# Performance work log

Measured on AMD Instinct MI355X. Metric: run time of the kernel, lower is better.

The kernel has to match this reference:

```python
import jax, jax.numpy as jnp
import numpy as np

SPATIAL_SHAPES = ((64, 64), (32, 32), (16, 16), (8, 8))  # (H_l, W_l) per level
N_HEADS, N_LEVELS, N_POINTS = 8, 4, 4
EMBED, HEAD_DIM = 256, 32


def _bilinear_sample(v_lvl, loc, H, W):
    """grid_sample(mode=bilinear, padding=zeros, align_corners=False).

    v_lvl: (B, nH, H*W, d)   loc: (B, Nq, nH, P, 2) with (x, y) in [0, 1].
    Returns (B, nH, Nq, P, d).
    """
    B, nH, _, d = v_lvl.shape
    Nq, P = loc.shape[1], loc.shape[3]
    g = 2.0 * loc - 1.0                      # normalized [-1, 1]
    px = ((g[..., 0] + 1.0) * W - 1.0) * 0.5  # pixel coords, align_corners=False
    py = ((g[..., 1] + 1.0) * H - 1.0) * 0.5
    x0 = jnp.floor(px); y0 = jnp.floor(py)
    wx = px - x0; wy = py - y0
    x0i = x0.astype(jnp.int32); y0i = y0.astype(jnp.int32)
    acc = jnp.zeros((B, nH, Nq * P, d), v_lvl.dtype)
    corners = ((0, 0, (1 - wx) * (1 - wy)), (1, 0, wx * (1 - wy)),
               (0, 1, (1 - wx) * wy), (1, 1, wx * wy))
    for dx, dy, w in corners:
        xi = x0i + dx; yi = y0i + dy
        valid = (xi >= 0) & (xi < W) & (yi >= 0) & (yi < H)
        idx = jnp.clip(yi, 0, H - 1) * W + jnp.clip(xi, 0, W - 1)  # (B,Nq,nH,P)
        idx_t = idx.transpose(0, 2, 1, 3).reshape(B, nH, Nq * P)
        wm = jnp.where(valid, w, 0.0).astype(v_lvl.dtype)
        wm = wm.transpose(0, 2, 1, 3).reshape(B, nH, Nq * P, 1)
        gathered = jnp.take_along_axis(v_lvl, idx_t[..., None], axis=2)
        acc = acc + wm * gathered
    return acc.reshape(B, nH, Nq, P, d)


def setup_inputs() -> dict:
    key = jax.random.key(0)
    ks = jax.random.split(key, 12)
    B, Nq = 4, sum(H * W for H, W in SPATIAL_SHAPES)
    Nv = Nq
    s = 1.0 / np.sqrt(EMBED)
    return {
        "query": jax.random.normal(ks[0], (B, Nq, EMBED), jnp.float32),
        "value": jax.random.normal(ks[1], (B, Nv, EMBED), jnp.float32),
        "reference_points": jax.random.uniform(ks[2], (B, Nq, N_LEVELS, 2), jnp.float32),
        "value_proj_w": jax.random.normal(ks[3], (EMBED, EMBED), jnp.float32) * s,
        "value_proj_b": jnp.zeros((EMBED,), jnp.float32),
        "offsets_w": jax.random.normal(ks[4], (EMBED, N_HEADS * N_LEVELS * N_POINTS * 2), jnp.float32) * (0.05 * s),
        "offsets_b": jax.random.normal(ks[5], (N_HEADS * N_LEVELS * N_POINTS * 2,), jnp.float32) * 2.0,
        "attn_w_w": jax.random.normal(ks[6], (EMBED, N_HEADS * N_LEVELS * N_POINTS), jnp.float32) * s,
        "attn_w_b": jnp.zeros((N_HEADS * N_LEVELS * N_POINTS,), jnp.float32),
        "out_w": jax.random.normal(ks[7], (EMBED, EMBED), jnp.float32) * s,
        "out_b": jnp.zeros((EMBED,), jnp.float32),
    }


def reference(query, value, reference_points, value_proj_w, value_proj_b,
              offsets_w, offsets_b, attn_w_w, attn_w_b, out_w, out_b):
    B, Nq, C = query.shape
    Nv = value.shape[1]
    v = (value @ value_proj_w + value_proj_b).reshape(B, Nv, N_HEADS, HEAD_DIM)
    off = (query @ offsets_w + offsets_b).reshape(B, Nq, N_HEADS, N_LEVELS, N_POINTS, 2)
    aw = (query @ attn_w_w + attn_w_b).reshape(B, Nq, N_HEADS, N_LEVELS * N_POINTS)
    aw = jax.nn.softmax(aw, axis=-1).reshape(B, Nq, N_HEADS, N_LEVELS, N_POINTS)
    norm = jnp.array([[W, H] for H, W in SPATIAL_SHAPES], dtype=query.dtype)  # (L,2) as (W,H)
    loc = reference_points[:, :, None, :, None, :] + off / norm[None, None, None, :, None, :]
    out = jnp.zeros((B, Nq, N_HEADS, HEAD_DIM), query.dtype)
    cursor = 0
    for l, (H, W) in enumerate(SPATIAL_SHAPES):
        v_lvl = v[:, cursor:cursor + H * W].transpose(0, 2, 1, 3)  # (B,nH,HW,d)
        cursor += H * W
        sampled = _bilinear_sample(v_lvl, loc[:, :, :, l], H, W)   # (B,nH,Nq,P,d)
        out = out + jnp.einsum('bnhp,bhnpd->bnhd', aw[:, :, :, l], sampled)
    return out.reshape(B, Nq, C) @ out_w + out_b
```

## Files before the change

kernel.cpp:

```cpp
#include <hip/hip_runtime.h>
#include <hip/hip_bf16.h>
#include <math.h>

#define B_ 4
#define NQ 5440
#define M_ROWS (B_ * NQ)
#define NH 8
#define NL 4
#define NP 4
#define HD 32

typedef __attribute__((ext_vector_type(8))) short bf16x8;
typedef __attribute__((ext_vector_type(4))) short bf16x4;
typedef __attribute__((ext_vector_type(4))) float f32x4;
typedef _Float16 f16;

static __device__ __forceinline__ unsigned short f2bf(float f) {
  union { float f; unsigned u; } v; v.f = f;
  unsigned r = (v.u + 0x7fffu + ((v.u >> 16) & 1u)) >> 16;
  return (unsigned short)r;
}
static __device__ __forceinline__ float bits2f(unsigned u) {
  union { unsigned u; float f; } v; v.u = u; return v.f;
}

__global__ __launch_bounds__(256) void prep_all(
    const float* __restrict__ value, const float* __restrict__ query,
    unsigned short* __restrict__ value_bf, unsigned short* __restrict__ query_bf,
    const float* __restrict__ vpw, const float* __restrict__ offw,
    const float* __restrict__ attnw, const float* __restrict__ outw,
    const float* __restrict__ offb, const float* __restrict__ attnb,
    unsigned short* __restrict__ vp_t, unsigned short* __restrict__ q_t,
    unsigned short* __restrict__ out_t, float* __restrict__ biasq, int n4) {
  int id = blockIdx.x * 256 + threadIdx.x;
  if (id < 2 * n4) {
    const float* src; unsigned short* dst; int j;
    if (id < n4) { src = value; dst = value_bf; j = id; }
    else { src = query; dst = query_bf; j = id - n4; }
    float4 f = ((const float4*)src)[j];
    bf16x4 o;
    o[0] = (short)f2bf(f.x); o[1] = (short)f2bf(f.y);
    o[2] = (short)f2bf(f.z); o[3] = (short)f2bf(f.w);
    ((bf16x4*)dst)[j] = o;
    return;
  }
  int w = id - 2 * n4;
  if (w < 65536) {
    int n = w >> 8, k = w & 255;
    vp_t[w] = f2bf(vpw[k * 256 + n]);
  } else if (w < 163840) {
    int q = w - 65536; int n = q >> 8, k = q & 255;
    q_t[q] = f2bf(n < 256 ? offw[k * 256 + n] : attnw[k * 128 + (n - 256)]);
  } else if (w < 229376) {
    int o = w - 163840; int n = o >> 8, k = o & 255;
    out_t[o] = f2bf(outw[k * 256 + n]);
  } else if (w < 229760) {
    int j = w - 229376;
    biasq[j] = j < 256 ? offb[j] : attnb[j - 256];
  }
}

__global__ __launch_bounds__(256) void gemm12_kernel(
    const unsigned short* __restrict__ valbf, const unsigned short* __restrict__ qrybf,
    const unsigned short* __restrict__ wt_vp, const unsigned short* __restrict__ wt_q,
    const float* __restrict__ vp_b, const float* __restrict__ biasq,
    unsigned short* __restrict__ v_bf, f16* __restrict__ offaw_h) {
  __shared__ unsigned short Bs[8 * 64 * 32];
  const int t = threadIdx.x;
  const int lane = t & 63, wid = t >> 6;
  const int qd = lane >> 4, l16 = lane & 15;
  const int g = blockIdx.x;
  const int grp = g / 80, r = g % 80;
  int by, bx;
  if (grp < 21) { by = grp * 8 + (r & 7); bx = r >> 3; }
  else          { by = 168 + (r & 1);     bx = r >> 1; }
  const int bm = by * 128;
  const bool isv = bx < 4;
  const int bn = isv ? bx * 64 : (bx - 4) * 64;
  const unsigned short* A  = isv ? valbf : qrybf;
  const unsigned short* Wt = isv ? wt_vp : wt_q;

  const unsigned short* bg = Wt + (size_t)(bn + (t >> 2)) * 256 + (t & 3) * 8;
  unsigned short* bs_b = Bs + (t & 192) * 8;
#pragma unroll
  for (int j = 0; j < 8; ++j)
    __builtin_amdgcn_global_load_lds(
        (const __attribute__((address_space(1))) void*)(bg + j * 32),
        (__attribute__((address_space(3))) void*)(bs_b + j * 2048), 16, 0, 0);

  const unsigned short* ar0 = A + (size_t)(bm + wid * 32 + l16) * 256 + qd * 8;
  const unsigned short* ar1 = ar0 + 16 * 256;
  bf16x8 a0[8], a1[8];
#pragma unroll
  for (int j = 0; j < 8; ++j) {
    a0[j] = *(const bf16x8*)(ar0 + j * 32);
    a1[j] = *(const bf16x8*)(ar1 + j * 32);
  }
  __syncthreads();

  f32x4 acc[2][4] = {};
#pragma unroll
  for (int j = 0; j < 8; ++j) {
    const unsigned short* bt = Bs + j * 2048 + l16 * 32 + qd * 8;
#pragma unroll
    for (int ni = 0; ni < 4; ++ni) {
      const bf16x8 bf = *(const bf16x8*)(bt + ni * 512);
      acc[0][ni] = __builtin_amdgcn_mfma_f32_16x16x32_bf16(a0[j], bf, acc[0][ni], 0, 0, 0);
      acc[1][ni] = __builtin_amdgcn_mfma_f32_16x16x32_bf16(a1[j], bf, acc[1][ni], 0, 0, 0);
    }
  }
  if (isv) {
#pragma unroll
    for (int ni = 0; ni < 4; ++ni) {
      const int c = bn + ni * 16 + l16;
      const float bb = vp_b[c];
      const int h = c >> 5, d = c & 31;
#pragma unroll
      for (int mi = 0; mi < 2; ++mi)
#pragma unroll
        for (int rr = 0; rr < 4; ++rr) {
          const int gm = bm + wid * 32 + mi * 16 + qd * 4 + rr;
          const int b = gm / NQ, pix = gm - b * NQ;
          v_bf[((size_t)(b * NH + h) * NQ + pix) * HD + d] = f2bf(acc[mi][ni][rr] + bb);
        }
    }
  } else {
#pragma unroll
    for (int ni = 0; ni < 4; ++ni) {
      const int c = bn + ni * 16 + l16;
      const float bb = biasq[c];
#pragma unroll
      for (int mi = 0; mi < 2; ++mi)
#pragma unroll
        for (int rr = 0; rr < 4; ++rr) {
          const int gm = bm + wid * 32 + mi * 16 + qd * 4 + rr;
          offaw_h[(size_t)gm * 384 + c] = (f16)(acc[mi][ni][rr] + bb);
        }
    }
  }
}

__global__ __launch_bounds__(256) void gemm_out_kernel(
    const unsigned short* __restrict__ attn_bf, const unsigned short* __restrict__ wt_out,
    const float* __restrict__ out_b, float* __restrict__ out) {
  __shared__ unsigned short Bs[8 * 64 * 32];
  const int t = threadIdx.x;
  const int lane = t & 63, wid = t >> 6;
  const int qd = lane >> 4, l16 = lane & 15;
  const int g = blockIdx.x;
  const int grp = g / 32, r = g % 32;
  int by, bx;
  if (grp < 21) { by = grp * 8 + (r & 7); bx = r >> 3; }
  else          { by = 168 + (r & 1);     bx = r >> 1; }
  const int bm = by * 128, bn = bx * 64;

  const unsigned short* bg = wt_out + (size_t)(bn + (t >> 2)) * 256 + (t & 3) * 8;
  unsigned short* bs_b = Bs + (t & 192) * 8;
#pragma unroll
  for (int j = 0; j < 8; ++j)
    __builtin_amdgcn_global_load_lds(
        (const __attribute__((address_space(1))) void*)(bg + j * 32),
        (__attribute__((address_space(3))) void*)(bs_b + j * 2048), 16, 0, 0);

  const unsigned short* ar0 = attn_bf + (size_t)(bm + wid * 32 + l16) * 256 + qd * 8;
  const unsigned short* ar1 = ar0 + 16 * 256;
  bf16x8 a0[8], a1[8];
#pragma unroll
  for (int j = 0; j < 8; ++j) {
    a0[j] = *(const bf16x8*)(ar0 + j * 32);
    a1[j] = *(const bf16x8*)(ar1 + j * 32);
  }
  __syncthreads();

  f32x4 acc[2][4] = {};
#pragma unroll
  for (int j = 0; j < 8; ++j) {
    const unsigned short* bt = Bs + j * 2048 + l16 * 32 + qd * 8;
#pragma unroll
    for (int ni = 0; ni < 4; ++ni) {
      const bf16x8 bf = *(const bf16x8*)(bt + ni * 512);
      acc[0][ni] = __builtin_amdgcn_mfma_f32_16x16x32_bf16(a0[j], bf, acc[0][ni], 0, 0, 0);
      acc[1][ni] = __builtin_amdgcn_mfma_f32_16x16x32_bf16(a1[j], bf, acc[1][ni], 0, 0, 0);
    }
  }
#pragma unroll
  for (int ni = 0; ni < 4; ++ni) {
    const int c = bn + ni * 16 + l16;
    const float bb = out_b[c];
#pragma unroll
    for (int mi = 0; mi < 2; ++mi)
#pragma unroll
      for (int rr = 0; rr < 4; ++rr) {
        const int gm = bm + wid * 32 + mi * 16 + qd * 4 + rr;
        out[(size_t)gm * 256 + c] = acc[mi][ni][rr] + bb;
      }
  }
}

__global__ __launch_bounds__(256) void sample_fused_kernel(
    const unsigned short* __restrict__ v, const float* __restrict__ refp,
    const f16* __restrict__ offaw_h, unsigned short* __restrict__ out) {
  __shared__ __align__(16) unsigned short s_idx[16 * 64 * 4];
  __shared__ __align__(16) float s_wts[16 * 64 * 4];
  const int t = threadIdx.x;
  const int blk = blockIdx.x;
  const int b = (blk & 7) >> 1;
  const int q0loc = ((blk >> 3) * 2 + (blk & 1)) * 8;
  const int q0 = b * NQ + q0loc;

  {
    const int lane = t & 63, wave = t >> 6;
    const int qh = wave * 16 + (lane >> 2);
    const int l = lane & 3;
    const int q = qh >> 3, h = qh & 7;
    const f16* row = offaw_h + (size_t)(q0 + q) * 384;
    union { uint4 u4; f16 hh[8]; } off8;
    off8.u4 = *(const uint4*)(row + h * 32 + l * 8);
    union { uint2 u2; f16 hh[4]; } lg4;
    lg4.u2 = *(const uint2*)(row + 256 + h * 16 + l * 4);
    const float2 rxy = *(const float2*)(refp + (size_t)(q0 + q) * 8 + l * 2);

    float lgf[4];
#pragma unroll
    for (int j = 0; j < 4; ++j) lgf[j] = (float)lg4.hh[j];
    float m = fmaxf(fmaxf(lgf[0], lgf[1]), fmaxf(lgf[2], lgf[3]));
    m = fmaxf(m, __shfl_xor(m, 1));
    m = fmaxf(m, __shfl_xor(m, 2));
    float e[4], s = 0.f;
#pragma unroll
    for (int j = 0; j < 4; ++j) { e[j] = __expf(lgf[j] - m); s += e[j]; }
    s += __shfl_xor(s, 1);
    s += __shfl_xor(s, 2);
    const float inv = 1.f / s;

    const int Wl = 64 >> l, Hl = 64 >> l;
    const float pxb = rxy.x * (float)Wl - 0.5f;
    const float pyb = rxy.y * (float)Hl - 0.5f;
#pragma unroll
    for (int pp = 0; pp < 4; ++pp) {
      const int p = l * 4 + pp;
      const float ox = (float)off8.hh[pp * 2];
      const float oy = (float)off8.hh[pp * 2 + 1];
      const float a  = e[pp] * inv;
      const float px = pxb + ox;
      const float py = pyb + oy;
      const float x0f = floorf(px), y0f = floorf(py);
      const int x0 = (int)x0f, y0 = (int)y0f;
      const int x1 = x0 + 1, y1 = y0 + 1;
      const float wx = px - x0f, wy = py - y0f;
      const float m_x0 = (x0 >= 0 && x0 < Wl) ? 1.f : 0.f;
      const float m_x1 = (x1 >= 0 && x1 < Wl) ? 1.f : 0.f;
      const float m_y0 = (y0 >= 0 && y0 < Hl) ? 1.f : 0.f;
      const float m_y1 = (y1 >= 0 && y1 < Hl) ? 1.f : 0.f;
      const int cx0 = min(max(x0, 0), Wl - 1), cx1 = min(max(x1, 0), Wl - 1);
      const int cy0 = min(max(y0, 0), Hl - 1), cy1 = min(max(y1, 0), Hl - 1);
      const int ti = (p * 64 + qh) * 4;
      ushort4 i4;
      i4.x = (unsigned short)(cy0 * Wl + cx0);
      i4.y = (unsigned short)(cy0 * Wl + cx1);
      i4.z = (unsigned short)(cy1 * Wl + cx0);
      i4.w = (unsigned short)(cy1 * Wl + cx1);
      float4 w4;
      w4.x = a * (1.f - wx) * (1.f - wy) * m_x0 * m_y0;
      w4.y = a * wx * (1.f - wy) * m_x1 * m_y0;
      w4.z = a * (1.f - wx) * wy * m_x0 * m_y1;
      w4.w = a * wx * wy * m_x1 * m_y1;
      *(ushort4*)&s_idx[ti] = i4;
      *(float4*)&s_wts[ti] = w4;
    }
  }
  __syncthreads();
  const int lane = t & 63, wave = t >> 6;
  const int qh_lo = lane >> 4;
  const int c     = (lane >> 2) & 3;
  const int d8    = lane & 3;
  const char* vB = (const char*)v;
  const unsigned bbase = (unsigned)(b * NH) * (unsigned)(NQ * 64) + (unsigned)(d8 * 16);

  for (int s = 0; s < 4; ++s) {
    const int tqh = wave * 16 + s * 4 + qh_lo;
    const int h = tqh & 7;
    const unsigned hb = bbase + (unsigned)h * (unsigned)(NQ * 64);
    float acc[8] = {};
#pragma unroll
    for (int l = 0; l < 4; ++l) {
      const unsigned LOFFB = (l == 0) ? 0u : (l == 1) ? 4096u * 64u
                           : (l == 2) ? 5120u * 64u : 5376u * 64u;
      const unsigned base = hb + LOFFB;
#pragma unroll
      for (int pp = 0; pp < 4; ++pp) {
        const int p = l * 4 + pp;
        const int ti = (p * 64 + tqh) * 4 + c;
        const unsigned idx = s_idx[ti];
        const float w = s_wts[ti];
        union { bf16x8 v8; unsigned u[4]; } cc;
        cc.v8 = *(const bf16x8*)(vB + base + (idx << 6));
#pragma unroll
        for (int k = 0; k < 4; ++k) {
          acc[2 * k]     += w * bits2f(cc.u[k] << 16);
          acc[2 * k + 1] += w * bits2f(cc.u[k] & 0xffff0000u);
        }
      }
    }
#pragma unroll
    for (int k = 0; k < 8; ++k) {
      acc[k] += __shfl_xor(acc[k], 4);
      acc[k] += __shfl_xor(acc[k], 8);
    }
    if (c == 0) {
      const int q = tqh >> 3;
      bf16x8 ov;
#pragma unroll
      for (int k = 0; k < 8; ++k) ov[k] = (short)f2bf(acc[k]);
      *(bf16x8*)(out + (size_t)(q0 + q) * 256 + h * HD + d8 * 8) = ov;
    }
  }
}

extern "C" void kernel_launch(void* const* d_in, const int* in_sizes, int n_in,
                              void* d_out, int out_size, void* d_ws, size_t ws_size,
                              hipStream_t stream) {
  const float* query        = (const float*)d_in[0];
  const float* value        = (const float*)d_in[1];
  const float* refp         = (const float*)d_in[2];
  const float* value_proj_w = (const float*)d_in[3];
  const float* value_proj_b = (const float*)d_in[4];
  const float* offsets_w    = (const float*)d_in[5];
  const float* offsets_b    = (const float*)d_in[6];
  const float* attn_w_w     = (const float*)d_in[7];
  const float* attn_w_b     = (const float*)d_in[8];
  const float* out_w        = (const float*)d_in[9];
  const float* out_b        = (const float*)d_in[10];
  float* out = (float*)d_out;

  const int M = M_ROWS;
  const size_t SZ_V   = (size_t)M * 256 * 2;
  const size_t SZ_OFF = (size_t)M * 384 * 2;
  char* w = (char*)d_ws;
  unsigned short* value_bf = (unsigned short*)w;
  unsigned short* attn_bf  = (unsigned short*)w;
  unsigned short* query_bf = (unsigned short*)(w + SZ_V);
  unsigned short* v_bf     = (unsigned short*)(w + 2 * SZ_V);
  f16* offaw_h             = (f16*)(w + 3 * SZ_V);
  char* wts                = w + 3 * SZ_V + SZ_OFF;
  unsigned short* wt_vp    = (unsigned short*)wts;
  unsigned short* wt_q     = wt_vp + 65536;
  unsigned short* wt_out   = wt_q + 98304;
  float* biasq             = (float*)(wt_out + 65536);

  dim3 blk(256);
  const int n4 = M * 64;
  const int prep_blocks = (2 * n4 + 229760 + 255) / 256;
  prep_all<<<prep_blocks, blk, 0, stream>>>(
      value, query, value_bf, query_bf,
      value_proj_w, offsets_w, attn_w_w, out_w, offsets_b, attn_w_b,
      wt_vp, wt_q, wt_out, biasq, n4);
  gemm12_kernel<<<1700, blk, 0, stream>>>(
      value_bf, query_bf, wt_vp, wt_q, value_proj_b, biasq, v_bf, offaw_h);
  sample_fused_kernel<<<M / 8, blk, 0, stream>>>(v_bf, refp, offaw_h, attn_bf);
  gemm_out_kernel<<<680, blk, 0, stream>>>(attn_bf, wt_out, out_b, out);
}
```

Measured before the change: 173.8 us.

## Add odd-shifted value copy so bilinear x-pairs load as one 128-byte fetch

Adds a kernel that builds a second copy of the projected value tensor in which horizontally adjacent pixel pairs starting at odd columns are stored contiguously. Together with the original layout, where even-aligned pairs are already adjacent, each bilinear sample's two x-neighbours can then be fetched from one 128-byte contiguous region, so the sampler stores two packed row indices per point instead of four. This is meant to cut gather transactions and shared-memory index traffic in the sampling kernel. In exchange it adds an extra kernel launch, about 11 MB of extra writes, and a larger workspace. It relies on hardcoded plane sizes and offsets.

```diff
diff --git a/kernel.cpp b/kernel.cpp
--- a/kernel.cpp
+++ b/kernel.cpp
@@ -9,6 +9,11 @@
 #define NL 4
 #define NP 4
 #define HD 32
+
+#define EV_PLANE 348160u
+#define OD_PLANE 363520u
+#define SZ_V_B   11141120u
+#define SZ_ODD_B 11632640u
 
 typedef __attribute__((ext_vector_type(8))) short bf16x8;
 typedef __attribute__((ext_vector_type(4))) short bf16x4;
@@ -140,67 +145,31 @@
   }
 }
 
-__global__ __launch_bounds__(256) void gemm_out_kernel(
-    const unsigned short* __restrict__ attn_bf, const unsigned short* __restrict__ wt_out,
-    const float* __restrict__ out_b, float* __restrict__ out) {
-  __shared__ unsigned short Bs[8 * 64 * 32];
-  const int t = threadIdx.x;
-  const int lane = t & 63, wid = t >> 6;
-  const int qd = lane >> 4, l16 = lane & 15;
-  const int g = blockIdx.x;
-  const int grp = g / 32, r = g % 32;
-  int by, bx;
-  if (grp < 21) { by = grp * 8 + (r & 7); bx = r >> 3; }
-  else          { by = 168 + (r & 1);     bx = r >> 1; }
-  const int bm = by * 128, bn = bx * 64;
-
-  const unsigned short* bg = wt_out + (size_t)(bn + (t >> 2)) * 256 + (t & 3) * 8;
-  unsigned short* bs_b = Bs + (t & 192) * 8;
-#pragma unroll
-  for (int j = 0; j < 8; ++j)
-    __builtin_amdgcn_global_load_lds(
-        (const __attribute__((address_space(1))) void*)(bg + j * 32),
-        (__attribute__((address_space(3))) void*)(bs_b + j * 2048), 16, 0, 0);
-
-  const unsigned short* ar0 = attn_bf + (size_t)(bm + wid * 32 + l16) * 256 + qd * 8;
-  const unsigned short* ar1 = ar0 + 16 * 256;
-  bf16x8 a0[8], a1[8];
-#pragma unroll
-  for (int j = 0; j < 8; ++j) {
-    a0[j] = *(const bf16x8*)(ar0 + j * 32);
-    a1[j] = *(const bf16x8*)(ar1 + j * 32);
-  }
-  __syncthreads();
-
-  f32x4 acc[2][4] = {};
-#pragma unroll
-  for (int j = 0; j < 8; ++j) {
-    const unsigned short* bt = Bs + j * 2048 + l16 * 32 + qd * 8;
-#pragma unroll
-    for (int ni = 0; ni < 4; ++ni) {
-      const bf16x8 bf = *(const bf16x8*)(bt + ni * 512);
-      acc[0][ni] = __builtin_amdgcn_mfma_f32_16x16x32_bf16(a0[j], bf, acc[0][ni], 0, 0, 0);
-      acc[1][ni] = __builtin_amdgcn_mfma_f32_16x16x32_bf16(a1[j], bf, acc[1][ni], 0, 0, 0);
-    }
-  }
-#pragma unroll
-  for (int ni = 0; ni < 4; ++ni) {
-    const int c = bn + ni * 16 + l16;
-    const float bb = out_b[c];
-#pragma unroll
-    for (int mi = 0; mi < 2; ++mi)
-#pragma unroll
-      for (int rr = 0; rr < 4; ++rr) {
-        const int gm = bm + wid * 32 + mi * 16 + qd * 4 + rr;
-        out[(size_t)gm * 256 + c] = acc[mi][ni][rr] + bb;
-      }
-  }
+__global__ __launch_bounds__(256) void dup_odd_kernel(
+    const unsigned short* __restrict__ v_even, unsigned short* __restrict__ v_odd) {
+  const int id = blockIdx.x * 256 + threadIdx.x;
+  const int pairglob = id >> 3;
+  const int half = (id >> 2) & 1, d8 = id & 3;
+  const int plane = pairglob / 2840;
+  const int r = pairglob - plane * 2840;
+  int l, row, k, Wl, loff;
+  if (r < 2112)      { l = 0; Wl = 64; loff = 0;    const int rr = r;        row = rr / 33; k = rr - row * 33; }
+  else if (r < 2656) { l = 1; Wl = 32; loff = 4096; const int rr = r - 2112; row = rr / 17; k = rr - row * 17; }
+  else if (r < 2800) { l = 2; Wl = 16; loff = 5120; const int rr = r - 2656; row = rr / 9;  k = rr - row * 9;  }
+  else               { l = 3; Wl = 8;  loff = 5376; const int rr = r - 2800; row = rr / 5;  k = rr - row * 5;  }
+  (void)l;
+  int px = 2 * k - 1 + half; px = min(max(px, 0), Wl - 1);
+  const int spix = loff + row * Wl + px;
+  const uint4 val = *(const uint4*)((const char*)v_even +
+      ((size_t)plane * 5440 + spix) * 64 + d8 * 16);
+  *(uint4*)((char*)v_odd + (size_t)plane * OD_PLANE + (size_t)r * 128 +
+            half * 64 + d8 * 16) = val;
 }
 
 __global__ __launch_bounds__(256) void sample_fused_kernel(
     const unsigned short* __restrict__ v, const float* __restrict__ refp,
     const f16* __restrict__ offaw_h, unsigned short* __restrict__ out) {
-  __shared__ __align__(16) unsigned short s_idx[16 * 64 * 4];
+  __shared__ __align__(16) unsigned s_idx32[16 * 64];
   __shared__ __align__(16) float s_wts[16 * 64 * 4];
   const int t = threadIdx.x;
   const int blk = blockIdx.x;
@@ -233,7 +202,9 @@
     s += __shfl_xor(s, 2);
     const float inv = 1.f / s;
 
-    const int Wl = 64 >> l, Hl = 64 >> l;
+    const int Wl = 64 >> l, Hl = 64 >> l, W2 = Wl >> 1;
+    const int EB = (l == 0) ? 0 : (l == 1) ? 2048 : (l == 2) ? 2560 : 2688;
+    const int OB = (l == 0) ? 0 : (l == 1) ? 2112 : (l == 2) ? 2656 : 2800;
     const float pxb = rxy.x * (float)Wl - 0.5f;
     const float pyb = rxy.y * (float)Hl - 0.5f;
 #pragma unroll
@@ -252,54 +223,50 @@
       const float m_x1 = (x1 >= 0 && x1 < Wl) ? 1.f : 0.f;
       const float m_y0 = (y0 >= 0 && y0 < Hl) ? 1.f : 0.f;
       const float m_y1 = (y1 >= 0 && y1 < Hl) ? 1.f : 0.f;
-      const int cx0 = min(max(x0, 0), Wl - 1), cx1 = min(max(x1, 0), Wl - 1);
       const int cy0 = min(max(y0, 0), Hl - 1), cy1 = min(max(y1, 0), Hl - 1);
-      const int ti = (p * 64 + qh) * 4;
-      ushort4 i4;
-      i4.x = (unsigned short)(cy0 * Wl + cx0);
-      i4.y = (unsigned short)(cy0 * Wl + cx1);
-      i4.z = (unsigned short)(cy1 * Wl + cx0);
-      i4.w = (unsigned short)(cy1 * Wl + cx1);
+      const int par = x0 & 1;
+      int col, base, rowp;
+      if (par) { col = min(max((x0 + 1) >> 1, 0), W2);     base = OB + 0x8000; rowp = W2 + 1; }
+      else     { col = min(max(x0 >> 1, 0), W2 - 1);       base = EB;          rowp = W2; }
+      const unsigned i0 = (unsigned)(base + cy0 * rowp + col);
+      const unsigned i1 = (unsigned)(base + cy1 * rowp + col);
+      const int ti = p * 64 + qh;
+      s_idx32[ti] = i0 | (i1 << 16);
       float4 w4;
       w4.x = a * (1.f - wx) * (1.f - wy) * m_x0 * m_y0;
       w4.y = a * wx * (1.f - wy) * m_x1 * m_y0;
       w4.z = a * (1.f - wx) * wy * m_x0 * m_y1;
       w4.w = a * wx * wy * m_x1 * m_y1;
-      *(ushort4*)&s_idx[ti] = i4;
-      *(float4*)&s_wts[ti] = w4;
+      *(float4*)&s_wts[ti * 4] = w4;
     }
   }
   __syncthreads();
   const int lane = t & 63, wave = t >> 6;
   const int qh_lo = lane >> 4;
-  const int c     = (lane >> 2) & 3;
+  const int rp    = (lane >> 3) & 1;
+  const int half  = (lane >> 2) & 1;
   const int d8    = lane & 3;
   const char* vB = (const char*)v;
-  const unsigned bbase = (unsigned)(b * NH) * (unsigned)(NQ * 64) + (unsigned)(d8 * 16);
+  const unsigned sub = (unsigned)(half * 64 + d8 * 16);
 
   for (int s = 0; s < 4; ++s) {
     const int tqh = wave * 16 + s * 4 + qh_lo;
     const int h = tqh & 7;
-    const unsigned hb = bbase + (unsigned)h * (unsigned)(NQ * 64);
+    const unsigned plane = (unsigned)(b * NH + h);
+    const unsigned ebase = plane * EV_PLANE + sub;
+    const unsigned obase = SZ_V_B + plane * OD_PLANE + sub;
     float acc[8] = {};
 #pragma unroll
-    for (int l = 0; l < 4; ++l) {
-      const unsigned LOFFB = (l == 0) ? 0u : (l == 1) ? 4096u * 64u
-                           : (l == 2) ? 5120u * 64u : 5376u * 64u;
-      const unsigned base = hb + LOFFB;
-#pragma unroll
-      for (int pp = 0; pp < 4; ++pp) {
-        const int p = l * 4 + pp;
-        const int ti = (p * 64 + tqh) * 4 + c;
-        const unsigned idx = s_idx[ti];
-        const float w = s_wts[ti];
-        union { bf16x8 v8; unsigned u[4]; } cc;
-        cc.v8 = *(const bf16x8*)(vB + base + (idx << 6));
-#pragma unroll
-        for (int k = 0; k < 4; ++k) {
-          acc[2 * k]     += w * bits2f(cc.u[k] << 16);
-          acc[2 * k + 1] += w * bits2f(cc.u[k] & 0xffff0000u);
-        }
+    for (int p = 0; p < 16; ++p) {
+      const unsigned ip = ((const unsigned short*)s_idx32)[(p * 64 + tqh) * 2 + rp];
+      const float w = s_wts[((p * 64 + tqh) * 2 + rp) * 2 + half];
+      const unsigned addr = ((ip & 0x8000u) ? obase : ebase) + ((ip & 0x7fffu) << 7);
+      union { bf16x8 v8; unsigned u[4]; } cc;
+      cc.v8 = *(const bf16x8*)(vB + addr);
+#pragma unroll
+      for (int k = 0; k < 4; ++k) {
+        acc[2 * k]     += w * bits2f(cc.u[k] << 16);
+        acc[2 * k + 1] += w * bits2f(cc.u[k] & 0xffff0000u);
       }
     }
 #pragma unroll
@@ -307,13 +274,70 @@
       acc[k] += __shfl_xor(acc[k], 4);
       acc[k] += __shfl_xor(acc[k], 8);
     }
-    if (c == 0) {
+    if ((lane & 12) == 0) {
       const int q = tqh >> 3;
       bf16x8 ov;
 #pragma unroll
       for (int k = 0; k < 8; ++k) ov[k] = (short)f2bf(acc[k]);
       *(bf16x8*)(out + (size_t)(q0 + q) * 256 + h * HD + d8 * 8) = ov;
     }
+  }
+}
+
+__global__ __launch_bounds__(256) void gemm_out_kernel(
+    const unsigned short* __restrict__ attn_bf, const unsigned short* __restrict__ wt_out,
+    const float* __restrict__ out_b, float* __restrict__ out) {
+  __shared__ unsigned short Bs[8 * 64 * 32];
+  const int t = threadIdx.x;
+  const int lane = t & 63, wid = t >> 6;
+  const int qd = lane >> 4, l16 = lane & 15;
+  const int g = blockIdx.x;
+  const int grp = g / 32, r = g % 32;
+  int by, bx;
+  if (grp < 21) { by = grp * 8 + (r & 7); bx = r >> 3; }
+  else          { by = 168 + (r & 1);     bx = r >> 1; }
+  const int bm = by * 128, bn = bx * 64;
+
+  const unsigned short* bg = wt_out + (size_t)(bn + (t >> 2)) * 256 + (t & 3) * 8;
+  unsigned short* bs_b = Bs + (t & 192) * 8;
+#pragma unroll
+  for (int j = 0; j < 8; ++j)
+    __builtin_amdgcn_global_load_lds(
+        (const __attribute__((address_space(1))) void*)(bg + j * 32),
+        (__attribute__((address_space(3))) void*)(bs_b + j * 2048), 16, 0, 0);
+
+  const unsigned short* ar0 = attn_bf + (size_t)(bm + wid * 32 + l16) * 256 + qd * 8;
+  const unsigned short* ar1 = ar0 + 16 * 256;
+  bf16x8 a0[8], a1[8];
+#pragma unroll
+  for (int j = 0; j < 8; ++j) {
+    a0[j] = *(const bf16x8*)(ar0 + j * 32);
+    a1[j] = *(const bf16x8*)(ar1 + j * 32);
+  }
+  __syncthreads();
+
+  f32x4 acc[2][4] = {};
+#pragma unroll
+  for (int j = 0; j < 8; ++j) {
+    const unsigned short* bt = Bs + j * 2048 + l16 * 32 + qd * 8;
+#pragma unroll
+    for (int ni = 0; ni < 4; ++ni) {
+      const bf16x8 bf = *(const bf16x8*)(bt + ni * 512);
+      acc[0][ni] = __builtin_amdgcn_mfma_f32_16x16x32_bf16(a0[j], bf, acc[0][ni], 0, 0, 0);
+      acc[1][ni] = __builtin_amdgcn_mfma_f32_16x16x32_bf16(a1[j], bf, acc[1][ni], 0, 0, 0);
+    }
+  }
+#pragma unroll
+  for (int ni = 0; ni < 4; ++ni) {
+    const int c = bn + ni * 16 + l16;
+    const float bb = out_b[c];
+#pragma unroll
+    for (int mi = 0; mi < 2; ++mi)
+#pragma unroll
+      for (int rr = 0; rr < 4; ++rr) {
+        const int gm = bm + wid * 32 + mi * 16 + qd * 4 + rr;
+        out[(size_t)gm * 256 + c] = acc[mi][ni][rr] + bb;
+      }
   }
 }
 
@@ -340,9 +364,10 @@
   unsigned short* value_bf = (unsigned short*)w;
   unsigned short* attn_bf  = (unsigned short*)w;
   unsigned short* query_bf = (unsigned short*)(w + SZ_V);
-  unsigned short* v_bf     = (unsigned short*)(w + 2 * SZ_V);
-  f16* offaw_h             = (f16*)(w + 3 * SZ_V);
-  char* wts                = w + 3 * SZ_V + SZ_OFF;
+  unsigned short* v_even   = (unsigned short*)(w + 2 * SZ_V);
+  unsigned short* v_odd    = (unsigned short*)(w + 3 * SZ_V);
+  f16* offaw_h             = (f16*)(w + 3 * SZ_V + SZ_ODD_B);
+  char* wts                = w + 3 * SZ_V + SZ_ODD_B + SZ_OFF;
   unsigned short* wt_vp    = (unsigned short*)wts;
   unsigned short* wt_q     = wt_vp + 65536;
   unsigned short* wt_out   = wt_q + 98304;
@@ -356,7 +381,8 @@
       value_proj_w, offsets_w, attn_w_w, out_w, offsets_b, attn_w_b,
       wt_vp, wt_q, wt_out, biasq, n4);
   gemm12_kernel<<<1700, blk, 0, stream>>>(
-      value_bf, query_bf, wt_vp, wt_q, value_proj_b, biasq, v_bf, offaw_h);
-  sample_fused_kernel<<<M / 8, blk, 0, stream>>>(v_bf, refp, offaw_h, attn_bf);
+      value_bf, query_bf, wt_vp, wt_q, value_proj_b, biasq, v_even, offaw_h);
+  dup_odd_kernel<<<2840, blk, 0, stream>>>(v_even, v_odd);
+  sample_fused_kernel<<<M / 8, blk, 0, stream>>>(v_even, refp, offaw_h, attn_bf);
   gemm_out_kernel<<<680, blk, 0, stream>>>(attn_bf, wt_out, out_b, out);
 }
```

New measurement: 179.7 us. 1.03x slower.
